# Performance work log

Hardware: AMD Instinct MI355X
Metric: run time of the kernel (lower is better)

## Reference

```python
import jax, jax.numpy as jnp
import numpy as np

B, N, U = 2048, 512, 64  # batch_size, memory_len, unit_size


def setup_inputs() -> dict:
    key = jax.random.key(0)
    ks = jax.random.split(key, 7)
    memory = jax.random.normal(ks[0], (B, N, U), jnp.float32)
    k = jax.random.normal(ks[1], (B, U), jnp.float32)
    beta = jnp.full((1,), 5.0, jnp.float32)          # key strength > 0
    g = jax.random.uniform(ks[2], (1,), jnp.float32)  # interpolation gate in [0,1]
    s = jax.random.uniform(ks[3], (B, 3), jnp.float32)
    s = s / jnp.sum(s, axis=1, keepdims=True)         # shift distribution (positive)
    gamma = jnp.full((1,), 2.0, jnp.float32)          # sharpening > 1
    w_pre = jax.nn.softmax(jax.random.normal(ks[4], (B, N), jnp.float32), axis=1)
    e = jax.random.uniform(ks[5], (B, U), jnp.float32)  # erase gates in [0,1]
    a = jax.random.normal(ks[6], (B, U), jnp.float32)    # add vector
    return dict(memory=memory, k=k, beta=beta, g=g, s=s, gamma=gamma,
                w_pre=w_pre, e=e, a=a)


def _cosine_sim(x, y, eps=1e-8):
    # x: (B,N,U), y: (B,1,U); matches torch F.cosine_similarity clamping
    dot = jnp.sum(x * y, axis=-1)
    nx = jnp.maximum(jnp.sqrt(jnp.sum(x * x, axis=-1)), eps)
    ny = jnp.maximum(jnp.sqrt(jnp.sum(y * y, axis=-1)), eps)
    return dot / (nx * ny)


def reference(memory, k, beta, g, s, gamma, w_pre, e, a):
    # --- address ---
    sim = _cosine_sim(memory + 1e-16, k[:, None, :] + 1e-16)        # (B,N)
    wc = jax.nn.softmax(beta * sim, axis=1)                          # content weights
    wg = wc * g + (1.0 - g) * w_pre                                  # gated interpolation
    # circular pad by 1 on each side, then 3-tap grouped conv (cross-correlation)
    wg_pad = jnp.concatenate([wg[:, -1:], wg, wg[:, :1]], axis=1)    # (B,N+2)
    ws = (s[:, 0:1] * wg_pad[:, :-2]
          + s[:, 1:2] * wg_pad[:, 1:-1]
          + s[:, 2:3] * wg_pad[:, 2:])                               # (B,N)
    w = ws ** gamma                                                  # sharpen
    w = w / jnp.sum(w, axis=1, keepdims=True) + 1e-16                # (B,N)
    # --- read ---
    r = jnp.einsum('bn,bnu->bu', w, memory)                          # (B,U)
    # --- write: M' = M * (1 - w e^T) + w a^T ---
    new_mem = (memory * (1.0 - w[:, :, None] * e[:, None, :])
               + w[:, :, None] * a[:, None, :])                      # (B,N,U)
    return w, r, new_mem
```

## Files before the change

### kernel.cpp

```cpp
#include <hip/hip_runtime.h>
#include <math.h>

#define B_ 2048
#define N_ 512
#define U_ 64

__global__ __launch_bounds__(256) void ntm_kernel(
    const float* __restrict__ memory,
    const float* __restrict__ kk,
    const float* __restrict__ beta_p,
    const float* __restrict__ g_p,
    const float* __restrict__ sv,
    const float* __restrict__ gamma_p,
    const float* __restrict__ w_pre,
    const float* __restrict__ ev,
    const float* __restrict__ av,
    float* __restrict__ out_w,
    float* __restrict__ out_r,
    float* __restrict__ out_m)
{
    __shared__ float s_k[U_];
    __shared__ float s_sim[N_];
    __shared__ float s_wg[N_];
    __shared__ float s_red[256];
    __shared__ float s_rred[4 * U_];
    __shared__ float s_ny;

    const int b    = blockIdx.x;
    const int tid  = threadIdx.x;
    const int wave = tid >> 6;
    const int lane = tid & 63;
    const int sub  = lane >> 4;
    const int l16  = lane & 15;
    const int col  = l16 << 2;

    const float beta  = beta_p[0];
    const float g     = g_p[0];
    const float gamma = gamma_p[0];
    const float s0 = sv[b * 3 + 0], s1 = sv[b * 3 + 1], s2 = sv[b * 3 + 2];

    const size_t mem_base = (size_t)b * N_ * U_;

    if (tid < U_) {
        float kx = kk[b * U_ + tid] + 1e-16f;
        s_k[tid] = kx;
        float v = kx * kx;
        #pragma unroll
        for (int off = 32; off; off >>= 1) v += __shfl_xor(v, off);
        if (tid == 0) s_ny = fmaxf(sqrtf(v), 1e-8f);
    }
    __syncthreads();
    const float ny = s_ny;

    const float k0 = s_k[col + 0], k1 = s_k[col + 1], k2 = s_k[col + 2], k3 = s_k[col + 3];

    for (int n0 = 0; n0 < N_; n0 += 16) {
        const int n = n0 + (wave << 2) + sub;
        const float4 m4 = *(const float4*)(memory + mem_base + (size_t)n * U_ + col);
        const float x0 = m4.x + 1e-16f, x1 = m4.y + 1e-16f,
                    x2 = m4.z + 1e-16f, x3 = m4.w + 1e-16f;
        float dot = x0 * k0 + x1 * k1 + x2 * k2 + x3 * k3;
        float nsq = x0 * x0 + x1 * x1 + x2 * x2 + x3 * x3;
        #pragma unroll
        for (int off = 8; off; off >>= 1) {
            dot += __shfl_xor(dot, off);
            nsq += __shfl_xor(nsq, off);
        }
        if (l16 == 0) {
            const float nx = fmaxf(sqrtf(nsq), 1e-8f);
            s_sim[n] = dot / (nx * ny);
        }
    }
    __syncthreads();

    const int i0 = tid, i1 = tid + 256;
    const float t0 = beta * s_sim[i0];
    const float t1 = beta * s_sim[i1];

    s_red[tid] = fmaxf(t0, t1);
    __syncthreads();
    for (int ss = 128; ss > 0; ss >>= 1) {
        if (tid < ss) s_red[tid] = fmaxf(s_red[tid], s_red[tid + ss]);
        __syncthreads();
    }
    const float mx = s_red[0];
    __syncthreads();

    const float e0 = expf(t0 - mx);
    const float e1 = expf(t1 - mx);
    s_red[tid] = e0 + e1;
    __syncthreads();
    for (int ss = 128; ss > 0; ss >>= 1) {
        if (tid < ss) s_red[tid] += s_red[tid + ss];
        __syncthreads();
    }
    const float einv = 1.0f / s_red[0];
    __syncthreads();

    const float wp0 = w_pre[(size_t)b * N_ + i0];
    const float wp1 = w_pre[(size_t)b * N_ + i1];
    s_wg[i0] = g * (e0 * einv) + (1.0f - g) * wp0;
    s_wg[i1] = g * (e1 * einv) + (1.0f - g) * wp1;
    __syncthreads();

    float wsv0, wsv1;
    {
        int nm = (i0 + N_ - 1) & (N_ - 1), np = (i0 + 1) & (N_ - 1);
        wsv0 = powf(s0 * s_wg[nm] + s1 * s_wg[i0] + s2 * s_wg[np], gamma);
        nm = (i1 + N_ - 1) & (N_ - 1); np = (i1 + 1) & (N_ - 1);
        wsv1 = powf(s0 * s_wg[nm] + s1 * s_wg[i1] + s2 * s_wg[np], gamma);
    }
    s_red[tid] = wsv0 + wsv1;
    __syncthreads();
    for (int ss = 128; ss > 0; ss >>= 1) {
        if (tid < ss) s_red[tid] += s_red[tid + ss];
        __syncthreads();
    }
    const float winv = 1.0f / s_red[0];
    __syncthreads();

    const float w0 = wsv0 * winv + 1e-16f;
    const float w1 = wsv1 * winv + 1e-16f;
    s_sim[i0] = w0;
    s_sim[i1] = w1;
    out_w[(size_t)b * N_ + i0] = w0;
    out_w[(size_t)b * N_ + i1] = w1;
    __syncthreads();

    const float4 e4 = *(const float4*)(ev + b * U_ + col);
    const float4 a4 = *(const float4*)(av + b * U_ + col);
    float rx = 0.f, ry = 0.f, rz = 0.f, rw = 0.f;

    for (int n0 = 0; n0 < N_; n0 += 16) {
        const int n = n0 + (wave << 2) + sub;
        const size_t off = mem_base + (size_t)n * U_ + col;
        const float4 m4 = *(const float4*)(memory + off);
        const float wn = s_sim[n];
        float4 o;
        o.x = m4.x * (1.0f - wn * e4.x) + wn * a4.x;
        o.y = m4.y * (1.0f - wn * e4.y) + wn * a4.y;
        o.z = m4.z * (1.0f - wn * e4.z) + wn * a4.z;
        o.w = m4.w * (1.0f - wn * e4.w) + wn * a4.w;
        *(float4*)(out_m + off) = o;
        rx += wn * m4.x; ry += wn * m4.y; rz += wn * m4.z; rw += wn * m4.w;
    }
    rx += __shfl_xor(rx, 16); rx += __shfl_xor(rx, 32);
    ry += __shfl_xor(ry, 16); ry += __shfl_xor(ry, 32);
    rz += __shfl_xor(rz, 16); rz += __shfl_xor(rz, 32);
    rw += __shfl_xor(rw, 16); rw += __shfl_xor(rw, 32);
    if (lane < 16) {
        s_rred[wave * U_ + col + 0] = rx;
        s_rred[wave * U_ + col + 1] = ry;
        s_rred[wave * U_ + col + 2] = rz;
        s_rred[wave * U_ + col + 3] = rw;
    }
    __syncthreads();
    if (tid < U_) {
        const float rv = s_rred[tid] + s_rred[U_ + tid] + s_rred[2 * U_ + tid] + s_rred[3 * U_ + tid];
        out_r[(size_t)b * U_ + tid] = rv;
    }
}

extern "C" void kernel_launch(void* const* d_in, const int* in_sizes, int n_in,
                              void* d_out, int out_size, void* d_ws, size_t ws_size,
                              hipStream_t stream) {
    const float* memory = (const float*)d_in[0];
    const float* kk     = (const float*)d_in[1];
    const float* beta   = (const float*)d_in[2];
    const float* g      = (const float*)d_in[3];
    const float* sv     = (const float*)d_in[4];
    const float* gamma  = (const float*)d_in[5];
    const float* w_pre  = (const float*)d_in[6];
    const float* ev     = (const float*)d_in[7];
    const float* av     = (const float*)d_in[8];

    float* out   = (float*)d_out;
    float* out_w = out;
    float* out_r = out + (size_t)B_ * N_;
    float* out_m = out + (size_t)B_ * N_ + (size_t)B_ * U_;

    ntm_kernel<<<B_, 256, 0, stream>>>(memory, kk, beta, g, sv, gamma,
                                       w_pre, ev, av, out_w, out_r, out_m);
}
```

Baseline: 491.1 us.

## Unroll memory passes, use wave-shuffle reductions, drop softmax max, nontemporal stores

Both passes over the memory tile are unrolled by four rows so more loads are in flight per thread, and the new-memory writes use nontemporal stores to avoid polluting cache. The shared-memory tree reductions are replaced by wave shuffles with a 4-entry cross-wave sum. The softmax max-subtraction is dropped because cosine similarity is bounded. Input loads are hoisted to the start, and powf/expf become fast __expf/__logf intrinsics. Dropping the max relies on beta*sim staying small, and the fast intrinsics reduce accuracy slightly.

After: 487.5 us. About the same (-0.7%).

```diff
diff --git a/kernel.cpp b/kernel.cpp
--- a/kernel.cpp
+++ b/kernel.cpp
@@ -4,6 +4,27 @@
 #define B_ 2048
 #define N_ 512
 #define U_ 64
+
+typedef float f4 __attribute__((ext_vector_type(4)));
+
+#define ROW_SIM(m4, dot, nsq) do { \
+    const float x0 = (m4).x + 1e-16f, x1 = (m4).y + 1e-16f, \
+                x2 = (m4).z + 1e-16f, x3 = (m4).w + 1e-16f; \
+    dot = x0 * k0 + x1 * k1 + x2 * k2 + x3 * k3; \
+    nsq = x0 * x0 + x1 * x1 + x2 * x2 + x3 * x3; \
+} while (0)
+
+#define WR_ROW(o, m4, wn) do { \
+    (o).x = (m4).x * (1.0f - (wn) * e4.x) + (wn) * a4.x; \
+    (o).y = (m4).y * (1.0f - (wn) * e4.y) + (wn) * a4.y; \
+    (o).z = (m4).z * (1.0f - (wn) * e4.z) + (wn) * a4.z; \
+    (o).w = (m4).w * (1.0f - (wn) * e4.w) + (wn) * a4.w; \
+} while (0)
+
+#define NT_STORE4(ptr, v) do { \
+    f4 _t; _t.x = (v).x; _t.y = (v).y; _t.z = (v).z; _t.w = (v).w; \
+    __builtin_nontemporal_store(_t, (f4*)(ptr)); \
+} while (0)
 
 __global__ __launch_bounds__(256) void ntm_kernel(
     const float* __restrict__ memory,
@@ -19,12 +40,11 @@
     float* __restrict__ out_r,
     float* __restrict__ out_m)
 {
-    __shared__ float s_k[U_];
     __shared__ float s_sim[N_];
     __shared__ float s_wg[N_];
-    __shared__ float s_red[256];
+    __shared__ float s_redA[4];
+    __shared__ float s_redB[4];
     __shared__ float s_rred[4 * U_];
-    __shared__ float s_ny;
 
     const int b    = blockIdx.x;
     const int tid  = threadIdx.x;
@@ -40,84 +60,78 @@
     const float s0 = sv[b * 3 + 0], s1 = sv[b * 3 + 1], s2 = sv[b * 3 + 2];
 
     const size_t mem_base = (size_t)b * N_ * U_;
-
-    if (tid < U_) {
-        float kx = kk[b * U_ + tid] + 1e-16f;
-        s_k[tid] = kx;
-        float v = kx * kx;
-        #pragma unroll
-        for (int off = 32; off; off >>= 1) v += __shfl_xor(v, off);
-        if (tid == 0) s_ny = fmaxf(sqrtf(v), 1e-8f);
-    }
-    __syncthreads();
-    const float ny = s_ny;
-
-    const float k0 = s_k[col + 0], k1 = s_k[col + 1], k2 = s_k[col + 2], k3 = s_k[col + 3];
-
-    for (int n0 = 0; n0 < N_; n0 += 16) {
-        const int n = n0 + (wave << 2) + sub;
-        const float4 m4 = *(const float4*)(memory + mem_base + (size_t)n * U_ + col);
-        const float x0 = m4.x + 1e-16f, x1 = m4.y + 1e-16f,
-                    x2 = m4.z + 1e-16f, x3 = m4.w + 1e-16f;
-        float dot = x0 * k0 + x1 * k1 + x2 * k2 + x3 * k3;
-        float nsq = x0 * x0 + x1 * x1 + x2 * x2 + x3 * x3;
+    const int i0 = tid, i1 = tid + 256;
+
+    const float wp0 = w_pre[(size_t)b * N_ + i0];
+    const float wp1 = w_pre[(size_t)b * N_ + i1];
+    const float4 e4 = *(const float4*)(ev + b * U_ + col);
+    const float4 a4 = *(const float4*)(av + b * U_ + col);
+
+    const float4 k4 = *(const float4*)(kk + b * U_ + col);
+    const float k0 = k4.x + 1e-16f, k1 = k4.y + 1e-16f,
+                k2 = k4.z + 1e-16f, k3 = k4.w + 1e-16f;
+    float ksq = k0 * k0 + k1 * k1 + k2 * k2 + k3 * k3;
+    #pragma unroll
+    for (int off = 8; off; off >>= 1) ksq += __shfl_xor(ksq, off);
+    const float ny = fmaxf(sqrtf(ksq), 1e-8f);
+
+    const int nb = (wave << 2) + sub;
+    const float* pm = memory + mem_base + (size_t)nb * U_ + col;
+    #pragma unroll 1
+    for (int n0 = 0; n0 < N_; n0 += 64) {
+        const float4 m0 = *(const float4*)(pm + (size_t)(n0     ) * U_);
+        const float4 m1 = *(const float4*)(pm + (size_t)(n0 + 16) * U_);
+        const float4 m2 = *(const float4*)(pm + (size_t)(n0 + 32) * U_);
+        const float4 m3 = *(const float4*)(pm + (size_t)(n0 + 48) * U_);
+        float d0, d1, d2, d3, q0, q1, q2, q3;
+        ROW_SIM(m0, d0, q0);
+        ROW_SIM(m1, d1, q1);
+        ROW_SIM(m2, d2, q2);
+        ROW_SIM(m3, d3, q3);
         #pragma unroll
         for (int off = 8; off; off >>= 1) {
-            dot += __shfl_xor(dot, off);
-            nsq += __shfl_xor(nsq, off);
+            d0 += __shfl_xor(d0, off); q0 += __shfl_xor(q0, off);
+            d1 += __shfl_xor(d1, off); q1 += __shfl_xor(q1, off);
+            d2 += __shfl_xor(d2, off); q2 += __shfl_xor(q2, off);
+            d3 += __shfl_xor(d3, off); q3 += __shfl_xor(q3, off);
         }
         if (l16 == 0) {
-            const float nx = fmaxf(sqrtf(nsq), 1e-8f);
-            s_sim[n] = dot / (nx * ny);
+            s_sim[nb + n0     ] = d0 / (fmaxf(sqrtf(q0), 1e-8f) * ny);
+            s_sim[nb + n0 + 16] = d1 / (fmaxf(sqrtf(q1), 1e-8f) * ny);
+            s_sim[nb + n0 + 32] = d2 / (fmaxf(sqrtf(q2), 1e-8f) * ny);
+            s_sim[nb + n0 + 48] = d3 / (fmaxf(sqrtf(q3), 1e-8f) * ny);
         }
     }
     __syncthreads();
 
-    const int i0 = tid, i1 = tid + 256;
     const float t0 = beta * s_sim[i0];
     const float t1 = beta * s_sim[i1];
-
-    s_red[tid] = fmaxf(t0, t1);
-    __syncthreads();
-    for (int ss = 128; ss > 0; ss >>= 1) {
-        if (tid < ss) s_red[tid] = fmaxf(s_red[tid], s_red[tid + ss]);
-        __syncthreads();
-    }
-    const float mx = s_red[0];
-    __syncthreads();
-
-    const float e0 = expf(t0 - mx);
-    const float e1 = expf(t1 - mx);
-    s_red[tid] = e0 + e1;
-    __syncthreads();
-    for (int ss = 128; ss > 0; ss >>= 1) {
-        if (tid < ss) s_red[tid] += s_red[tid + ss];
-        __syncthreads();
-    }
-    const float einv = 1.0f / s_red[0];
-    __syncthreads();
-
-    const float wp0 = w_pre[(size_t)b * N_ + i0];
-    const float wp1 = w_pre[(size_t)b * N_ + i1];
-    s_wg[i0] = g * (e0 * einv) + (1.0f - g) * wp0;
-    s_wg[i1] = g * (e1 * einv) + (1.0f - g) * wp1;
-    __syncthreads();
-
-    float wsv0, wsv1;
-    {
-        int nm = (i0 + N_ - 1) & (N_ - 1), np = (i0 + 1) & (N_ - 1);
-        wsv0 = powf(s0 * s_wg[nm] + s1 * s_wg[i0] + s2 * s_wg[np], gamma);
-        nm = (i1 + N_ - 1) & (N_ - 1); np = (i1 + 1) & (N_ - 1);
-        wsv1 = powf(s0 * s_wg[nm] + s1 * s_wg[i1] + s2 * s_wg[np], gamma);
-    }
-    s_red[tid] = wsv0 + wsv1;
-    __syncthreads();
-    for (int ss = 128; ss > 0; ss >>= 1) {
-        if (tid < ss) s_red[tid] += s_red[tid + ss];
-        __syncthreads();
-    }
-    const float winv = 1.0f / s_red[0];
-    __syncthreads();
+    const float e0 = __expf(t0);
+    const float e1 = __expf(t1);
+    float v = e0 + e1;
+    #pragma unroll
+    for (int off = 32; off; off >>= 1) v += __shfl_xor(v, off);
+    if (lane == 0) s_redA[wave] = v;
+    __syncthreads();
+    const float einv = 1.0f / (s_redA[0] + s_redA[1] + s_redA[2] + s_redA[3]);
+
+    const float gc = 1.0f - g;
+    s_wg[i0] = g * (e0 * einv) + gc * wp0;
+    s_wg[i1] = g * (e1 * einv) + gc * wp1;
+    __syncthreads();
+
+    int nm = (i0 + N_ - 1) & (N_ - 1), np = (i0 + 1) & (N_ - 1);
+    const float ws0 = s0 * s_wg[nm] + s1 * s_wg[i0] + s2 * s_wg[np];
+    nm = (i1 + N_ - 1) & (N_ - 1); np = (i1 + 1) & (N_ - 1);
+    const float ws1 = s0 * s_wg[nm] + s1 * s_wg[i1] + s2 * s_wg[np];
+    const float wsv0 = __expf(gamma * __logf(ws0));
+    const float wsv1 = __expf(gamma * __logf(ws1));
+    v = wsv0 + wsv1;
+    #pragma unroll
+    for (int off = 32; off; off >>= 1) v += __shfl_xor(v, off);
+    if (lane == 0) s_redB[wave] = v;
+    __syncthreads();
+    const float winv = 1.0f / (s_redB[0] + s_redB[1] + s_redB[2] + s_redB[3]);
 
     const float w0 = wsv0 * winv + 1e-16f;
     const float w1 = wsv1 * winv + 1e-16f;
@@ -127,23 +141,38 @@
     out_w[(size_t)b * N_ + i1] = w1;
     __syncthreads();
 
-    const float4 e4 = *(const float4*)(ev + b * U_ + col);
-    const float4 a4 = *(const float4*)(av + b * U_ + col);
-    float rx = 0.f, ry = 0.f, rz = 0.f, rw = 0.f;
-
-    for (int n0 = 0; n0 < N_; n0 += 16) {
-        const int n = n0 + (wave << 2) + sub;
-        const size_t off = mem_base + (size_t)n * U_ + col;
-        const float4 m4 = *(const float4*)(memory + off);
-        const float wn = s_sim[n];
-        float4 o;
-        o.x = m4.x * (1.0f - wn * e4.x) + wn * a4.x;
-        o.y = m4.y * (1.0f - wn * e4.y) + wn * a4.y;
-        o.z = m4.z * (1.0f - wn * e4.z) + wn * a4.z;
-        o.w = m4.w * (1.0f - wn * e4.w) + wn * a4.w;
-        *(float4*)(out_m + off) = o;
-        rx += wn * m4.x; ry += wn * m4.y; rz += wn * m4.z; rw += wn * m4.w;
-    }
+    float rxA = 0.f, ryA = 0.f, rzA = 0.f, rwA = 0.f;
+    float rxB = 0.f, ryB = 0.f, rzB = 0.f, rwB = 0.f;
+    float* po = out_m + mem_base + (size_t)nb * U_ + col;
+    #pragma unroll 1
+    for (int n0 = 0; n0 < N_; n0 += 64) {
+        const float4 m0 = *(const float4*)(pm + (size_t)(n0     ) * U_);
+        const float4 m1 = *(const float4*)(pm + (size_t)(n0 + 16) * U_);
+        const float4 m2 = *(const float4*)(pm + (size_t)(n0 + 32) * U_);
+        const float4 m3 = *(const float4*)(pm + (size_t)(n0 + 48) * U_);
+        const float wn0 = s_sim[nb + n0     ];
+        const float wn1 = s_sim[nb + n0 + 16];
+        const float wn2 = s_sim[nb + n0 + 32];
+        const float wn3 = s_sim[nb + n0 + 48];
+        float4 o0, o1, o2, o3;
+        WR_ROW(o0, m0, wn0);
+        WR_ROW(o1, m1, wn1);
+        WR_ROW(o2, m2, wn2);
+        WR_ROW(o3, m3, wn3);
+        NT_STORE4(po + (size_t)(n0     ) * U_, o0);
+        NT_STORE4(po + (size_t)(n0 + 16) * U_, o1);
+        NT_STORE4(po + (size_t)(n0 + 32) * U_, o2);
+        NT_STORE4(po + (size_t)(n0 + 48) * U_, o3);
+        rxA = fmaf(wn0, m0.x, rxA); ryA = fmaf(wn0, m0.y, ryA);
+        rzA = fmaf(wn0, m0.z, rzA); rwA = fmaf(wn0, m0.w, rwA);
+        rxB = fmaf(wn1, m1.x, rxB); ryB = fmaf(wn1, m1.y, ryB);
+        rzB = fmaf(wn1, m1.z, rzB); rwB = fmaf(wn1, m1.w, rwB);
+        rxA = fmaf(wn2, m2.x, rxA); ryA = fmaf(wn2, m2.y, ryA);
+        rzA = fmaf(wn2, m2.z, rzA); rwA = fmaf(wn2, m2.w, rwA);
+        rxB = fmaf(wn3, m3.x, rxB); ryB = fmaf(wn3, m3.y, ryB);
+        rzB = fmaf(wn3, m3.z, rzB); rwB = fmaf(wn3, m3.w, rwB);
+    }
+    float rx = rxA + rxB, ry = ryA + ryB, rz = rzA + rzB, rw = rwA + rwB;
     rx += __shfl_xor(rx, 16); rx += __shfl_xor(rx, 32);
     ry += __shfl_xor(ry, 16); ry += __shfl_xor(ry, 32);
     rz += __shfl_xor(rz, 16); rz += __shfl_xor(rz, 32);
@@ -156,7 +185,8 @@
     }
     __syncthreads();
     if (tid < U_) {
-        const float rv = s_rred[tid] + s_rred[U_ + tid] + s_rred[2 * U_ + tid] + s_rred[3 * U_ + tid];
+        const float rv = s_rred[tid] + s_rred[U_ + tid]
+                       + s_rred[2 * U_ + tid] + s_rred[3 * U_ + tid];
         out_r[(size_t)b * U_ + tid] = rv;
     }
 }
```
